# Optimization experiments

Hardware: AMD Instinct MI355X
Metric: run time of the kernel (lower is better)

Reference implementation:

```python
import jax, jax.numpy as jnp
import numpy as np

EPS = 1e-6
DIAG_SIZE = 128  # triu band half-width (init kwarg diag_size)
NEG_INF = -1e9


def feature_map(x):
    # tanh feature map: phi(x) = tanh(x) + 1 (positive feature map)
    return jnp.tanh(x) + 1.0


def causal_dot_product(Q, K, V):
    # Q,K: [N,L,H,E], V: [N,L,H,D]
    # running KV state: S_l = sum_{s<=l} K_s V_s^T, materialized via cumsum
    kv = jnp.cumsum(jnp.einsum('nlhe,nlhd->nlhed', K, V), axis=1)  # [N,L,H,E,D]
    return jnp.einsum('nlhe,nlhed->nlhd', Q, kv)


def setup_inputs() -> dict:
    key = jax.random.key(0)
    k1, k2, k3 = jax.random.split(key, 3)
    N, L, H, E = 2, 2048, 8, 64
    queries = jax.random.normal(k1, (N, L, H, E), dtype=jnp.float32)
    keys = jax.random.normal(k2, (N, L, H, E), dtype=jnp.float32)
    values = jax.random.normal(k3, (N, L, H, E), dtype=jnp.float32)
    key_lengths_mask = jnp.ones((N, L), dtype=jnp.float32)  # all keys valid
    blend = jnp.full((1,), 0.9, dtype=jnp.float32)  # learned blend param (init 0.9)
    return {"queries": queries, "keys": keys, "values": values,
            "key_lengths_mask": key_lengths_mask, "blend": blend}


def reference(queries, keys, values, key_lengths_mask, blend):
    N, L, H, E = queries.shape
    # ---- linear attention path (kernel_1 = tanh, kernel_2 = 'none') ----
    Q1 = feature_map(queries)
    K1 = feature_map(keys) * key_lengths_mask[:, :, None, None]
    Z1 = 1.0 / (jnp.einsum('nlhi,nlhi->nlh', Q1, jnp.cumsum(K1, axis=1)) + EPS)
    LV = causal_dot_product(Q1, K1, values) * Z1[..., None]  # [N,L,H,D]
    # ---- full softmax attention path (banded by triu) ----
    softmax_temp = 1.0 / np.sqrt(E).astype(np.float32)
    QK = jnp.einsum('nlhe,nshe->nhls', queries, keys)  # [N,H,L,L]
    l_idx = jnp.arange(L)[:, None]
    s_idx = jnp.arange(L)[None, :]
    causal_add = jnp.where(s_idx <= l_idx, 0.0, NEG_INF)  # lower-triangular mask
    key_add = jnp.where(key_lengths_mask > 0, 0.0, NEG_INF)  # [N,L]
    logits = softmax_temp * (QK + causal_add[None, None] + key_add[:, None, None, :])
    A = jax.nn.softmax(logits, axis=-1)
    # torch.triu(A, diagonal=-diag_size): keep s >= l - diag_size
    band = s_idx >= (l_idx - DIAG_SIZE)
    A = jnp.where(band[None, None], A, 0.0)
    # dropout: eval mode (identity)
    SV = jnp.einsum('nhls,nshd->nlhd', A, values)
    b = blend[0]
    return b * SV + (1.0 - b) * LV
```

## Files before the change

kernel.cpp:

```cpp
#include <hip/hip_runtime.h>
#include <math.h>

#define N_ 2
#define L_ 2048
#define H_ 8
#define E_ 64
#define D_ 64
#define C_ 128
#define NC (L_/C_)
#define ROWSTRIDE (H_*E_)
#define TEMP 0.125f
#define EPS_F 1e-6f
#define NEG_INF_F (-1e9f)
#define CHUNK_WS (E_*D_ + E_)
#define NCHUNKS (N_*H_*NC)
#define TPAD 136
#define PPAD 72

typedef __attribute__((ext_vector_type(8))) short short8;
typedef __attribute__((ext_vector_type(4))) float f32x4;

__device__ __forceinline__ short f2bf(float x) {
  unsigned u = __float_as_uint(x);
  u += 0x7fffu + ((u >> 16) & 1u);
  return (short)(u >> 16);
}
__device__ __forceinline__ float bf2f(short s) {
  return __uint_as_float(((unsigned)(unsigned short)s) << 16);
}
__device__ __forceinline__ float tanh1f(float x) {
  float e = __expf(-2.f * x);
  return 2.f * __builtin_amdgcn_rcpf(1.f + e);
}

template <int RS, typename F>
__device__ __forceinline__ void load_tile(float* __restrict__ dst,
                                          const float* __restrict__ src_base,
                                          F f) {
  const int t = threadIdx.x;
#pragma unroll
  for (int k = 0; k < 8; ++k) {
    int idx4 = k * 256 + t;
    int s = idx4 >> 4;
    int e = (idx4 & 15) << 2;
    float4 v = *(const float4*)(src_base + s * ROWSTRIDE + e);
    v = f(v, s);
    *(float4*)(dst + s * RS + e) = v;
  }
}

__device__ __forceinline__ void load_bf16_tile(short* __restrict__ dst,
                                               const float* __restrict__ src) {
  const int t = threadIdx.x;
#pragma unroll
  for (int it = 0; it < 4; ++it) {
    int gi = it * 256 + t;
    int row = gi >> 3, g = gi & 7;
    const float* p = src + row * ROWSTRIDE + g * 8;
    float4 a = *(const float4*)p;
    float4 b = *(const float4*)(p + 4);
    short8 v;
    v[0] = f2bf(a.x); v[1] = f2bf(a.y); v[2] = f2bf(a.z); v[3] = f2bf(a.w);
    v[4] = f2bf(b.x); v[5] = f2bf(b.y); v[6] = f2bf(b.z); v[7] = f2bf(b.w);
    int sg = g ^ (row & 7);
    *(short8*)(dst + row * 64 + sg * 8) = v;
  }
}

__device__ __forceinline__ short8 frag_ld(const short* __restrict__ buf,
                                          int rowbase, int hf, int lane) {
  int r = rowbase + (lane & 15);
  int g = (hf * 4 + (lane >> 4)) ^ (r & 7);
  return *(const short8*)(buf + r * 64 + g * 8);
}
__device__ __forceinline__ short8 frag_ldT(const short* __restrict__ buf,
                                           int nbase, int g, int lane) {
  int r = nbase + (lane & 15);
  return *(const short8*)(buf + r * TPAD + g * 8);
}
__device__ __forceinline__ short8 frag_ldP(const short* __restrict__ buf,
                                           int rowbase, int ks, int lane) {
  int r = rowbase + (lane & 15);
  int g = ks * 4 + (lane >> 4);
  return *(const short8*)(buf + r * PPAD + g * 8);
}

extern "C" __global__ void __launch_bounds__(256)
k_chunksums(const float* __restrict__ K, const float* __restrict__ V,
            const float* __restrict__ mask, float* __restrict__ ws) {
  __shared__ float kbuf[C_ * E_];
  __shared__ float vbuf[C_ * E_];
  const int orig = blockIdx.x;
  const int swz = (orig & 7) * 32 + (orig >> 3);
  const int c = swz & (NC - 1), nh = swz >> 4, h = nh & (H_ - 1), n = nh >> 3;
  const int t = threadIdx.x;
  const int gbase = ((n * L_ + c * C_) * H_ + h) * E_;
  const float* mrow = mask + n * L_ + c * C_;

  load_tile<E_>(kbuf, K + gbase, [&](float4 v, int s) {
    float km = mrow[s];
    v.x = tanh1f(v.x) * km; v.y = tanh1f(v.y) * km;
    v.z = tanh1f(v.z) * km; v.w = tanh1f(v.w) * km;
    return v;
  });
  load_tile<E_>(vbuf, V + gbase, [&](float4 v, int) { return v; });
  __syncthreads();

  const int e0 = (t >> 4) << 2, d0 = (t & 15) << 2;
  float acc[4][4] = {};
  for (int s = 0; s < C_; ++s) {
    float4 kk = *(const float4*)(kbuf + s * E_ + e0);
    float4 vv = *(const float4*)(vbuf + s * E_ + d0);
    float ka[4] = {kk.x, kk.y, kk.z, kk.w};
    float va[4] = {vv.x, vv.y, vv.z, vv.w};
#pragma unroll
    for (int a = 0; a < 4; ++a)
#pragma unroll
      for (int b = 0; b < 4; ++b) acc[a][b] += ka[a] * va[b];
  }
  float* wsc = ws + (size_t)(nh * NC + c) * CHUNK_WS;
#pragma unroll
  for (int a = 0; a < 4; ++a) {
    float4 st = {acc[a][0], acc[a][1], acc[a][2], acc[a][3]};
    *(float4*)(wsc + (e0 + a) * D_ + d0) = st;
  }
  if (t < E_) {
    float sum = 0.f;
    for (int s = 0; s < C_; ++s) sum += kbuf[s * E_ + t];
    wsc[E_ * D_ + t] = sum;
  }
}

extern "C" __global__ void __launch_bounds__(256)
k_scan(float* __restrict__ ws) {
  const int bid = blockIdx.x;
  const int swz = (bid & 7) * 34 + (bid >> 3);
  const int nh = swz / 17, seg = swz - nh * 17;
  const int idx = seg * 256 + threadIdx.x;
  if (idx >= CHUNK_WS) return;
  float* base = ws + (size_t)nh * NC * CHUNK_WS + idx;
  float v[NC];
#pragma unroll
  for (int c = 0; c < NC; ++c) v[c] = base[(size_t)c * CHUNK_WS];
  float acc = 0.f;
#pragma unroll
  for (int c = 0; c < NC; ++c) {
    base[(size_t)c * CHUNK_WS] = acc;
    acc += v[c];
  }
}

extern "C" __global__ void __launch_bounds__(256)
k_denom(const float* __restrict__ Q, const float* __restrict__ K,
        const float* __restrict__ mask, float* __restrict__ part) {
  __shared__ short qlds[C_ * E_];
  __shared__ short klds[C_ * E_];
  __shared__ float kmsk[C_];
  const int orig = blockIdx.x;
  const int swz = (orig & 7) * 272 + (orig >> 3);
  const int nh = swz / 136;
  const int p = swz - nh * 136;
  int qb = (int)((sqrtf(8.f * p + 1.f) - 1.f) * 0.5f);
  while ((qb + 1) * (qb + 2) / 2 <= p) ++qb;
  while (qb * (qb + 1) / 2 > p) --qb;
  const int kb = p - qb * (qb + 1) / 2;
  const int h = nh & (H_ - 1), n = nh >> 3;
  const int t = threadIdx.x;

  load_bf16_tile(qlds, Q + ((n * L_ + qb * C_) * H_ + h) * E_);
  load_bf16_tile(klds, K + ((n * L_ + kb * C_) * H_ + h) * E_);
  if (t < C_) kmsk[t] = mask[n * L_ + kb * C_ + t];
  __syncthreads();

  const int w = t >> 6, lane = t & 63;
  const int rowbase = w * 32;

  short8 afr[2][2];
#pragma unroll
  for (int m = 0; m < 2; ++m)
#pragma unroll
    for (int hh = 0; hh < 2; ++hh)
      afr[m][hh] = frag_ld(qlds, rowbase + 16 * m, hh, lane);

  f32x4 acc[2][8];
#pragma unroll
  for (int m = 0; m < 2; ++m)
#pragma unroll
    for (int c = 0; c < 8; ++c) acc[m][c] = (f32x4){0.f, 0.f, 0.f, 0.f};

#pragma unroll
  for (int c = 0; c < 8; ++c) {
    short8 b0 = frag_ld(klds, 16 * c, 0, lane);
    short8 b1 = frag_ld(klds, 16 * c, 1, lane);
#pragma unroll
    for (int m = 0; m < 2; ++m) {
      acc[m][c] = __builtin_amdgcn_mfma_f32_16x16x32_bf16(afr[m][0], b0, acc[m][c], 0, 0, 0);
      acc[m][c] = __builtin_amdgcn_mfma_f32_16x16x32_bf16(afr[m][1], b1, acc[m][c], 0, 0, 0);
    }
  }

  const bool diag = (kb == qb);
  const int col_lo = lane & 15;
  float* pout = part + (size_t)(nh * NC + qb) * C_ * 16;
#pragma unroll
  for (int m = 0; m < 2; ++m) {
    const int rbase = rowbase + 16 * m + (lane >> 4) * 4;
    float rs[4] = {0.f, 0.f, 0.f, 0.f};
#pragma unroll
    for (int c = 0; c < 8; ++c) {
      const int col = 16 * c + col_lo;
      const float madd = (kmsk[col] > 0.f) ? 0.f : NEG_INF_F;
#pragma unroll
      for (int reg = 0; reg < 4; ++reg) {
        float x = acc[m][c][reg] + madd;
        if (diag && col > rbase + reg) x += NEG_INF_F;
        rs[reg] += __expf(x * TEMP);
      }
    }
#pragma unroll
    for (int off = 1; off < 16; off <<= 1) {
#pragma unroll
      for (int reg = 0; reg < 4; ++reg) rs[reg] += __shfl_xor(rs[reg], off);
    }
    if (col_lo == 0) {
#pragma unroll
      for (int reg = 0; reg < 4; ++reg) pout[(rbase + reg) * 16 + kb] = rs[reg];
    }
  }
}

extern "C" __global__ void __launch_bounds__(256, 2)
k_fused(const float* __restrict__ Q, const float* __restrict__ K,
        const float* __restrict__ V, const float* __restrict__ mask,
        const float* __restrict__ blend, const float* __restrict__ ws,
        const float* __restrict__ part, float* __restrict__ out) {
  __shared__ short qs[64 * 64];
  __shared__ short q1[64 * 64];
  __shared__ short kA[C_ * 64];
  __shared__ short kB[C_ * 64];
  __shared__ short kv[64 * TPAD];
  __shared__ short pbuf[64 * PPAD];
  __shared__ float zlds[64];
  __shared__ float dinv[64];
  __shared__ float ksum[E_];
  __shared__ float kmskC[C_];
  __shared__ float kmskP[C_];

  const int orig = blockIdx.x;
  const int swz = (orig & 7) * 64 + (orig >> 3);
  const int rh = swz & 1, qb = (swz >> 1) & (NC - 1), nh = swz >> 5;
  const int h = nh & (H_ - 1), n = nh >> 3;
  const int t = threadIdx.x;
  const int w = t >> 6, lane = t & 63;
  const int rowbase = w * 16;
  const int col_lo = lane & 15;
  const int rb = rowbase + ((lane >> 4) << 2);
  const int rtile0 = rh * 64 + rb;
  const int qgbase = ((n * L_ + qb * C_ + rh * 64) * H_ + h) * E_;
  const int kbase_chunk = ((n * L_ + qb * C_) * H_ + h) * E_;
  const float* wsc = ws + (size_t)(nh * NC + qb) * CHUNK_WS;
  const float bl = blend[0];
  const float ob = 1.f - bl;

#pragma unroll
  for (int it = 0; it < 2; ++it) {
    int gi = it * 256 + t, row = gi >> 3, g = gi & 7;
    const float* p = Q + qgbase + row * ROWSTRIDE + g * 8;
    float4 a = *(const float4*)p, b = *(const float4*)(p + 4);
    float xs[8] = {a.x, a.y, a.z, a.w, b.x, b.y, b.z, b.w};
    short8 vs, v1;
#pragma unroll
    for (int j = 0; j < 8; ++j) { vs[j] = f2bf(xs[j]); v1[j] = f2bf(tanh1f(xs[j])); }
    int sg = g ^ (row & 7);
    *(short8*)(qs + row * 64 + sg * 8) = vs;
    *(short8*)(q1 + row * 64 + sg * 8) = v1;
  }
  {
    const float* mrow = mask + n * L_ + qb * C_;
#pragma unroll
    for (int it = 0; it < 4; ++it) {
      int gi = it * 256 + t, row = gi >> 3, g = gi & 7;
      const float* p = K + kbase_chunk + row * ROWSTRIDE + g * 8;
      float4 a = *(const float4*)p, b = *(const float4*)(p + 4);
      float km = mrow[row];
      float xs[8] = {a.x, a.y, a.z, a.w, b.x, b.y, b.z, b.w};
      short8 vr, v1;
#pragma unroll
      for (int j = 0; j < 8; ++j) { vr[j] = f2bf(xs[j]); v1[j] = f2bf(tanh1f(xs[j]) * km); }
      int sg = g ^ (row & 7);
      *(short8*)(kB + row * 64 + sg * 8) = vr;
      *(short8*)(kA + row * 64 + sg * 8) = v1;
    }
  }
  {
    int d = t & 63, eb = t >> 6;
#pragma unroll
    for (int q = 0; q < 2; ++q) {
      int e0 = eb * 16 + q * 8;
      short8 v;
#pragma unroll
      for (int j = 0; j < 8; ++j) v[j] = f2bf(wsc[(e0 + j) * D_ + d]);
      *(short8*)(kv + d * TPAD + (e0 >> 3) * 8) = v;
    }
  }
  float vcur[32];
  {
    int d = t & 63, sb = t >> 6;
#pragma unroll
    for (int q = 0; q < 4; ++q)
#pragma unroll
      for (int j = 0; j < 8; ++j)
        vcur[q * 8 + j] = V[kbase_chunk + (sb * 32 + q * 8 + j) * ROWSTRIDE + d];
  }
  if (t < E_) ksum[t] = wsc[E_ * D_ + t];
  if (t < C_) kmskC[t] = mask[n * L_ + qb * C_ + t];
  if (t < 64) {
    const float* pb = part + ((size_t)(nh * NC + qb) * C_ + rh * 64 + t) * 16;
    float4 a = *(const float4*)pb, b = *(const float4*)(pb + 4);
    float4 c = *(const float4*)(pb + 8), d4 = *(const float4*)(pb + 12);
    float vv[16] = {a.x, a.y, a.z, a.w, b.x, b.y, b.z, b.w,
                    c.x, c.y, c.z, c.w, d4.x, d4.y, d4.z, d4.w};
    float s = 0.f;
#pragma unroll
    for (int j = 0; j < 16; ++j) s += (j <= qb) ? vv[j] : 0.f;
    dinv[t] = 1.f / s;
  }
  __syncthreads();

  short8 af1[2], afs[2];
#pragma unroll
  for (int kh = 0; kh < 2; ++kh) {
    af1[kh] = frag_ld(q1, rowbase, kh, lane);
    afs[kh] = frag_ld(qs, rowbase, kh, lane);
  }
  f32x4 c1[8];
#pragma unroll
  for (int ct = 0; ct < 8; ++ct) c1[ct] = (f32x4){0.f, 0.f, 0.f, 0.f};
#pragma unroll
  for (int ct = 0; ct < 8; ++ct) {
    short8 b0 = frag_ld(kA, 16 * ct, 0, lane);
    short8 b1 = frag_ld(kA, 16 * ct, 1, lane);
    c1[ct] = __builtin_amdgcn_mfma_f32_16x16x32_bf16(af1[0], b0, c1[ct], 0, 0, 0);
    c1[ct] = __builtin_amdgcn_mfma_f32_16x16x32_bf16(af1[1], b1, c1[ct], 0, 0, 0);
  }
  if (t < 64) {
    float zz = 0.f;
#pragma unroll
    for (int gg = 0; gg < 8; ++gg) {
      int g = (gg + (t >> 3)) & 7;
      short8 v = *(const short8*)(q1 + t * 64 + ((g ^ (t & 7)) * 8));
#pragma unroll
      for (int j = 0; j < 8; ++j) zz += bf2f(v[j]) * ksum[g * 8 + j];
    }
    zlds[t] = zz;
  }
  float rs[4] = {0.f, 0.f, 0.f, 0.f};
#pragma unroll
  for (int ct = 0; ct < 8; ++ct) {
    int col = 16 * ct + col_lo;
#pragma unroll
    for (int reg = 0; reg < 4; ++reg) {
      if (col <= rtile0 + reg) rs[reg] += c1[ct][reg];
      else c1[ct][reg] = 0.f;
    }
  }
#pragma unroll
  for (int off = 1; off < 16; off <<= 1)
#pragma unroll
    for (int reg = 0; reg < 4; ++reg) rs[reg] += __shfl_xor(rs[reg], off);

  f32x4 accL[4];
#pragma unroll
  for (int nn = 0; nn < 4; ++nn) accL[nn] = (f32x4){0.f, 0.f, 0.f, 0.f};
#pragma unroll
  for (int ks = 0; ks < 2; ++ks) {
    short8 bf[4];
#pragma unroll
    for (int nn = 0; nn < 4; ++nn)
      bf[nn] = frag_ldT(kv, 16 * nn, ks * 4 + (lane >> 4), lane);
#pragma unroll
    for (int nn = 0; nn < 4; ++nn)
      accL[nn] = __builtin_amdgcn_mfma_f32_16x16x32_bf16(af1[ks], bf[nn], accL[nn], 0, 0, 0);
  }
  __syncthreads();

  {
    int d = t & 63, sb = t >> 6;
#pragma unroll
    for (int q = 0; q < 4; ++q) {
      short8 v;
#pragma unroll
      for (int j = 0; j < 8; ++j) v[j] = f2bf(vcur[q * 8 + j]);
      *(short8*)(kv + d * TPAD + ((sb * 32 + q * 8) >> 3) * 8) = v;
    }
  }
  __syncthreads();

  const bool haveprev = (qb > 0);
  const int kgp = ((n * L_ + (qb - 1) * C_) * H_ + h) * E_;
  float vpre[32];
  if (haveprev) {
    int d = t & 63, sb = t >> 6;
#pragma unroll
    for (int q = 0; q < 4; ++q)
#pragma unroll
      for (int j = 0; j < 8; ++j)
        vpre[q * 8 + j] = V[kgp + (sb * 32 + q * 8 + j) * ROWSTRIDE + d];
  }
#pragma unroll
  for (int hh = 0; hh < 2; ++hh) {
#pragma unroll
    for (int ch = 0; ch < 4; ++ch) {
      int ct = 4 * hh + ch, colh = 16 * ch + col_lo;
#pragma unroll
      for (int reg = 0; reg < 4; ++reg)
        pbuf[(rb + reg) * PPAD + colh] = f2bf(c1[ct][reg]);
    }
#pragma unroll
    for (int ks = 0; ks < 2; ++ks) {
      short8 ap = frag_ldP(pbuf, rowbase, ks, lane);
      short8 bv[4];
#pragma unroll
      for (int nn = 0; nn < 4; ++nn)
        bv[nn] = frag_ldT(kv, 16 * nn, 8 * hh + ks * 4 + (lane >> 4), lane);
#pragma unroll
      for (int nn = 0; nn < 4; ++nn)
        accL[nn] = __builtin_amdgcn_mfma_f32_16x16x32_bf16(ap, bv[nn], accL[nn], 0, 0, 0);
    }
  }
  f32x4 accS[4];
#pragma unroll
  for (int nn = 0; nn < 4; ++nn) accS[nn] = (f32x4){0.f, 0.f, 0.f, 0.f};
  {
    f32x4 cs[8];
#pragma unroll
    for (int ct = 0; ct < 8; ++ct) cs[ct] = (f32x4){0.f, 0.f, 0.f, 0.f};
#pragma unroll
    for (int ct = 0; ct < 8; ++ct) {
      short8 b0 = frag_ld(kB, 16 * ct, 0, lane);
      short8 b1 = frag_ld(kB, 16 * ct, 1, lane);
      cs[ct] = __builtin_amdgcn_mfma_f32_16x16x32_bf16(afs[0], b0, cs[ct], 0, 0, 0);
      cs[ct] = __builtin_amdgcn_mfma_f32_16x16x32_bf16(afs[1], b1, cs[ct], 0, 0, 0);
    }
#pragma unroll
    for (int ct = 0; ct < 8; ++ct) {
      int col = 16 * ct + col_lo;
      float madd = (kmskC[col] > 0.f) ? 0.f : NEG_INF_F;
#pragma unroll
      for (int reg = 0; reg < 4; ++reg) {
        float x = cs[ct][reg] + madd;
        if (col > rtile0 + reg) x += NEG_INF_F;
        cs[ct][reg] = __expf(x * TEMP);
      }
    }
#pragma unroll
    for (int hh = 0; hh < 2; ++hh) {
#pragma unroll
      for (int ch = 0; ch < 4; ++ch) {
        int ct = 4 * hh + ch, colh = 16 * ch + col_lo;
#pragma unroll
        for (int reg = 0; reg < 4; ++reg)
          pbuf[(rb + reg) * PPAD + colh] = f2bf(cs[ct][reg]);
      }
#pragma unroll
      for (int ks = 0; ks < 2; ++ks) {
        short8 ap = frag_ldP(pbuf, rowbase, ks, lane);
        short8 bv[4];
#pragma unroll
        for (int nn = 0; nn < 4; ++nn)
          bv[nn] = frag_ldT(kv, 16 * nn, 8 * hh + ks * 4 + (lane >> 4), lane);
#pragma unroll
        for (int nn = 0; nn < 4; ++nn)
          accS[nn] = __builtin_amdgcn_mfma_f32_16x16x32_bf16(ap, bv[nn], accS[nn], 0, 0, 0);
      }
    }
  }

  if (haveprev) {
    __syncthreads();
#pragma unroll
    for (int it = 0; it < 4; ++it) {
      int gi = it * 256 + t, row = gi >> 3, g = gi & 7;
      const float* p = K + kgp + row * ROWSTRIDE + g * 8;
      float4 a = *(const float4*)p, b = *(const float4*)(p + 4);
      short8 vr;
      vr[0] = f2bf(a.x); vr[1] = f2bf(a.y); vr[2] = f2bf(a.z); vr[3] = f2bf(a.w);
      vr[4] = f2bf(b.x); vr[5] = f2bf(b.y); vr[6] = f2bf(b.z); vr[7] = f2bf(b.w);
      int sg = g ^ (row & 7);
      *(short8*)(kA + row * 64 + sg * 8) = vr;
    }
    {
      int d = t & 63, sb = t >> 6;
#pragma unroll
      for (int q = 0; q < 4; ++q) {
        short8 v;
#pragma unroll
        for (int j = 0; j < 8; ++j) v[j] = f2bf(vpre[q * 8 + j]);
        *(short8*)(kv + d * TPAD + ((sb * 32 + q * 8) >> 3) * 8) = v;
      }
    }
    if (t < C_) kmskP[t] = mask[n * L_ + (qb - 1) * C_ + t];
    __syncthreads();

    f32x4 cs[8];
#pragma unroll
    for (int ct = 0; ct < 8; ++ct) cs[ct] = (f32x4){0.f, 0.f, 0.f, 0.f};
#pragma unroll
    for (int ct = 0; ct < 8; ++ct) {
      short8 b0 = frag_ld(kA, 16 * ct, 0, lane);
      short8 b1 = frag_ld(kA, 16 * ct, 1, lane);
      cs[ct] = __builtin_amdgcn_mfma_f32_16x16x32_bf16(afs[0], b0, cs[ct], 0, 0, 0);
      cs[ct] = __builtin_amdgcn_mfma_f32_16x16x32_bf16(afs[1], b1, cs[ct], 0, 0, 0);
    }
#pragma unroll
    for (int ct = 0; ct < 8; ++ct) {
      int col = 16 * ct + col_lo;
      float madd = (kmskP[col] > 0.f) ? 0.f : NEG_INF_F;
#pragma unroll
      for (int reg = 0; reg < 4; ++reg) {
        float x = cs[ct][reg] + madd;
        float pp = __expf(x * TEMP);
        if (col < rtile0 + reg) pp = 0.f;
        cs[ct][reg] = pp;
      }
    }
#pragma unroll
    for (int hh = 0; hh < 2; ++hh) {
#pragma unroll
      for (int ch = 0; ch < 4; ++ch) {
        int ct = 4 * hh + ch, colh = 16 * ch + col_lo;
#pragma unroll
        for (int reg = 0; reg < 4; ++reg)
          pbuf[(rb + reg) * PPAD + colh] = f2bf(cs[ct][reg]);
      }
#pragma unroll
      for (int ks = 0; ks < 2; ++ks) {
        short8 ap = frag_ldP(pbuf, rowbase, ks, lane);
        short8 bv[4];
#pragma unroll
        for (int nn = 0; nn < 4; ++nn)
          bv[nn] = frag_ldT(kv, 16 * nn, 8 * hh + ks * 4 + (lane >> 4), lane);
#pragma unroll
        for (int nn = 0; nn < 4; ++nn)
          accS[nn] = __builtin_amdgcn_mfma_f32_16x16x32_bf16(ap, bv[nn], accS[nn], 0, 0, 0);
      }
    }
  }

  float zrf[4], sdv[4];
#pragma unroll
  for (int reg = 0; reg < 4; ++reg) {
    zrf[reg] = ob / (zlds[rb + reg] + rs[reg] + EPS_F);
    sdv[reg] = bl * dinv[rb + reg];
  }
#pragma unroll
  for (int nn = 0; nn < 4; ++nn)
#pragma unroll
    for (int reg = 0; reg < 4; ++reg)
      out[qgbase + (rb + reg) * ROWSTRIDE + 16 * nn + col_lo] =
          zrf[reg] * accL[nn][reg] + sdv[reg] * accS[nn][reg];
}

extern "C" void kernel_launch(void* const* d_in, const int* in_sizes, int n_in,
                              void* d_out, int out_size, void* d_ws, size_t ws_size,
                              hipStream_t stream) {
  (void)in_sizes; (void)n_in; (void)out_size; (void)ws_size;
  const float* Q = (const float*)d_in[0];
  const float* K = (const float*)d_in[1];
  const float* V = (const float*)d_in[2];
  const float* mask = (const float*)d_in[3];
  const float* blend = (const float*)d_in[4];
  float* out = (float*)d_out;
  float* ws = (float*)d_ws;
  float* part = ws + (size_t)NCHUNKS * CHUNK_WS;

  k_denom<<<dim3(N_ * H_ * 136), dim3(256), 0, stream>>>(Q, K, mask, part);
  k_chunksums<<<dim3(N_ * H_ * NC), dim3(256), 0, stream>>>(K, V, mask, ws);
  k_scan<<<dim3(272), dim3(256), 0, stream>>>(ws);
  k_fused<<<dim3(N_ * H_ * NC * 2), dim3(256), 0, stream>>>(Q, K, V, mask, blend, ws, part, out);
}
```

Measured before the change: 49.10 us.

## Merge denom and chunk-sum kernels; MFMA chunk sums; cut LDS in fused kernel

```diff
diff --git a/kernel.cpp b/kernel.cpp
--- a/kernel.cpp
+++ b/kernel.cpp
@@ -33,22 +33,6 @@
   return 2.f * __builtin_amdgcn_rcpf(1.f + e);
 }
 
-template <int RS, typename F>
-__device__ __forceinline__ void load_tile(float* __restrict__ dst,
-                                          const float* __restrict__ src_base,
-                                          F f) {
-  const int t = threadIdx.x;
-#pragma unroll
-  for (int k = 0; k < 8; ++k) {
-    int idx4 = k * 256 + t;
-    int s = idx4 >> 4;
-    int e = (idx4 & 15) << 2;
-    float4 v = *(const float4*)(src_base + s * ROWSTRIDE + e);
-    v = f(v, s);
-    *(float4*)(dst + s * RS + e) = v;
-  }
-}
-
 __device__ __forceinline__ void load_bf16_tile(short* __restrict__ dst,
                                                const float* __restrict__ src) {
   const int t = threadIdx.x;
@@ -85,49 +69,136 @@
   return *(const short8*)(buf + r * PPAD + g * 8);
 }
 
-extern "C" __global__ void __launch_bounds__(256)
-k_chunksums(const float* __restrict__ K, const float* __restrict__ V,
-            const float* __restrict__ mask, float* __restrict__ ws) {
-  __shared__ float kbuf[C_ * E_];
-  __shared__ float vbuf[C_ * E_];
+extern "C" __global__ void __launch_bounds__(256, 4)
+k_pre(const float* __restrict__ Q, const float* __restrict__ K,
+      const float* __restrict__ V, const float* __restrict__ mask,
+      float* __restrict__ ws, float* __restrict__ part) {
+  __shared__ short ldsA[64 * TPAD];
+  __shared__ short ldsB[64 * TPAD];
+  __shared__ float fmsk[C_];
   const int orig = blockIdx.x;
-  const int swz = (orig & 7) * 32 + (orig >> 3);
-  const int c = swz & (NC - 1), nh = swz >> 4, h = nh & (H_ - 1), n = nh >> 3;
+  const int swz = (orig & 7) * 304 + (orig >> 3);
   const int t = threadIdx.x;
-  const int gbase = ((n * L_ + c * C_) * H_ + h) * E_;
-  const float* mrow = mask + n * L_ + c * C_;
-
-  load_tile<E_>(kbuf, K + gbase, [&](float4 v, int s) {
-    float km = mrow[s];
-    v.x = tanh1f(v.x) * km; v.y = tanh1f(v.y) * km;
-    v.z = tanh1f(v.z) * km; v.w = tanh1f(v.w) * km;
-    return v;
-  });
-  load_tile<E_>(vbuf, V + gbase, [&](float4 v, int) { return v; });
-  __syncthreads();
-
-  const int e0 = (t >> 4) << 2, d0 = (t & 15) << 2;
-  float acc[4][4] = {};
-  for (int s = 0; s < C_; ++s) {
-    float4 kk = *(const float4*)(kbuf + s * E_ + e0);
-    float4 vv = *(const float4*)(vbuf + s * E_ + d0);
-    float ka[4] = {kk.x, kk.y, kk.z, kk.w};
-    float va[4] = {vv.x, vv.y, vv.z, vv.w};
-#pragma unroll
-    for (int a = 0; a < 4; ++a)
-#pragma unroll
-      for (int b = 0; b < 4; ++b) acc[a][b] += ka[a] * va[b];
-  }
-  float* wsc = ws + (size_t)(nh * NC + c) * CHUNK_WS;
-#pragma unroll
-  for (int a = 0; a < 4; ++a) {
-    float4 st = {acc[a][0], acc[a][1], acc[a][2], acc[a][3]};
-    *(float4*)(wsc + (e0 + a) * D_ + d0) = st;
-  }
-  if (t < E_) {
-    float sum = 0.f;
-    for (int s = 0; s < C_; ++s) sum += kbuf[s * E_ + t];
-    wsc[E_ * D_ + t] = sum;
+  const int w = t >> 6, lane = t & 63;
+  const int col_lo = lane & 15;
+
+  if (swz < 2176) {
+    const int nh = swz / 136;
+    const int p = swz - nh * 136;
+    int qb = (int)((sqrtf(8.f * p + 1.f) - 1.f) * 0.5f);
+    while ((qb + 1) * (qb + 2) / 2 <= p) ++qb;
+    while (qb * (qb + 1) / 2 > p) --qb;
+    const int kb = p - qb * (qb + 1) / 2;
+    const int h = nh & (H_ - 1), n = nh >> 3;
+
+    load_bf16_tile(ldsA, Q + ((n * L_ + qb * C_) * H_ + h) * E_);
+    load_bf16_tile(ldsB, K + ((n * L_ + kb * C_) * H_ + h) * E_);
+    if (t < C_) fmsk[t] = mask[n * L_ + kb * C_ + t];
+    __syncthreads();
+
+    const int rowbase = w * 32;
+    short8 afr[2][2];
+#pragma unroll
+    for (int m = 0; m < 2; ++m)
+#pragma unroll
+      for (int hh = 0; hh < 2; ++hh)
+        afr[m][hh] = frag_ld(ldsA, rowbase + 16 * m, hh, lane);
+
+    f32x4 acc[2][8];
+#pragma unroll
+    for (int m = 0; m < 2; ++m)
+#pragma unroll
+      for (int c = 0; c < 8; ++c) acc[m][c] = (f32x4){0.f, 0.f, 0.f, 0.f};
+
+#pragma unroll
+    for (int c = 0; c < 8; ++c) {
+      short8 b0 = frag_ld(ldsB, 16 * c, 0, lane);
+      short8 b1 = frag_ld(ldsB, 16 * c, 1, lane);
+#pragma unroll
+      for (int m = 0; m < 2; ++m) {
+        acc[m][c] = __builtin_amdgcn_mfma_f32_16x16x32_bf16(afr[m][0], b0, acc[m][c], 0, 0, 0);
+        acc[m][c] = __builtin_amdgcn_mfma_f32_16x16x32_bf16(afr[m][1], b1, acc[m][c], 0, 0, 0);
+      }
+    }
+
+    const bool diag = (kb == qb);
+    float* pout = part + (size_t)(nh * NC + qb) * C_ * 16;
+#pragma unroll
+    for (int m = 0; m < 2; ++m) {
+      const int rbase = rowbase + 16 * m + (lane >> 4) * 4;
+      float rs[4] = {0.f, 0.f, 0.f, 0.f};
+#pragma unroll
+      for (int c = 0; c < 8; ++c) {
+        const int col = 16 * c + col_lo;
+        const float madd = (fmsk[col] > 0.f) ? 0.f : NEG_INF_F;
+#pragma unroll
+        for (int reg = 0; reg < 4; ++reg) {
+          float x = acc[m][c][reg] + madd;
+          if (diag && col > rbase + reg) x += NEG_INF_F;
+          rs[reg] += __expf(x * TEMP);
+        }
+      }
+#pragma unroll
+      for (int off = 1; off < 16; off <<= 1) {
+#pragma unroll
+        for (int reg = 0; reg < 4; ++reg) rs[reg] += __shfl_xor(rs[reg], off);
+      }
+      if (col_lo == 0) {
+#pragma unroll
+        for (int reg = 0; reg < 4; ++reg) pout[(rbase + reg) * 16 + kb] = rs[reg];
+      }
+    }
+  } else {
+    const int id = swz - 2176;
+    const int nh = id >> 4, c = id & 15;
+    const int h = nh & (H_ - 1), n = nh >> 3;
+    const int gbase = ((n * L_ + c * C_) * H_ + h) * E_;
+    const int e = t & 63, sb = t >> 6;
+    const int mbase = n * L_ + c * C_;
+#pragma unroll
+    for (int q = 0; q < 4; ++q) {
+      int s0 = sb * 32 + q * 8;
+      short8 kk, vv;
+#pragma unroll
+      for (int j = 0; j < 8; ++j) {
+        float kx = K[gbase + (s0 + j) * ROWSTRIDE + e];
+        kk[j] = f2bf(tanh1f(kx) * mask[mbase + s0 + j]);
+        vv[j] = f2bf(V[gbase + (s0 + j) * ROWSTRIDE + e]);
+      }
+      *(short8*)(ldsA + e * TPAD + (s0 >> 3) * 8) = kk;
+      *(short8*)(ldsB + e * TPAD + (s0 >> 3) * 8) = vv;
+    }
+    __syncthreads();
+
+    f32x4 acc[4];
+#pragma unroll
+    for (int nn = 0; nn < 4; ++nn) acc[nn] = (f32x4){0.f, 0.f, 0.f, 0.f};
+#pragma unroll
+    for (int ks = 0; ks < 4; ++ks) {
+      short8 a = frag_ldT(ldsB, 16 * w, ks * 4 + (lane >> 4), lane);
+#pragma unroll
+      for (int nn = 0; nn < 4; ++nn) {
+        short8 b = frag_ldT(ldsA, 16 * nn, ks * 4 + (lane >> 4), lane);
+        acc[nn] = __builtin_amdgcn_mfma_f32_16x16x32_bf16(a, b, acc[nn], 0, 0, 0);
+      }
+    }
+    float* wsc = ws + (size_t)(nh * NC + c) * CHUNK_WS;
+    const int drow = 16 * w + ((lane >> 4) << 2);
+#pragma unroll
+    for (int nn = 0; nn < 4; ++nn)
+#pragma unroll
+      for (int reg = 0; reg < 4; ++reg)
+        wsc[(16 * nn + col_lo) * D_ + drow + reg] = acc[nn][reg];
+    if (t < 64) {
+      float s = 0.f;
+#pragma unroll
+      for (int g = 0; g < 16; ++g) {
+        short8 v = *(const short8*)(ldsA + t * TPAD + g * 8);
+#pragma unroll
+        for (int j = 0; j < 8; ++j) s += bf2f(v[j]);
+      }
+      wsc[E_ * D_ + t] = s;
+    }
   }
 }
 
@@ -150,94 +221,12 @@
   }
 }
 
-extern "C" __global__ void __launch_bounds__(256)
-k_denom(const float* __restrict__ Q, const float* __restrict__ K,
-        const float* __restrict__ mask, float* __restrict__ part) {
-  __shared__ short qlds[C_ * E_];
-  __shared__ short klds[C_ * E_];
-  __shared__ float kmsk[C_];
-  const int orig = blockIdx.x;
-  const int swz = (orig & 7) * 272 + (orig >> 3);
-  const int nh = swz / 136;
-  const int p = swz - nh * 136;
-  int qb = (int)((sqrtf(8.f * p + 1.f) - 1.f) * 0.5f);
-  while ((qb + 1) * (qb + 2) / 2 <= p) ++qb;
-  while (qb * (qb + 1) / 2 > p) --qb;
-  const int kb = p - qb * (qb + 1) / 2;
-  const int h = nh & (H_ - 1), n = nh >> 3;
-  const int t = threadIdx.x;
-
-  load_bf16_tile(qlds, Q + ((n * L_ + qb * C_) * H_ + h) * E_);
-  load_bf16_tile(klds, K + ((n * L_ + kb * C_) * H_ + h) * E_);
-  if (t < C_) kmsk[t] = mask[n * L_ + kb * C_ + t];
-  __syncthreads();
-
-  const int w = t >> 6, lane = t & 63;
-  const int rowbase = w * 32;
-
-  short8 afr[2][2];
-#pragma unroll
-  for (int m = 0; m < 2; ++m)
-#pragma unroll
-    for (int hh = 0; hh < 2; ++hh)
-      afr[m][hh] = frag_ld(qlds, rowbase + 16 * m, hh, lane);
-
-  f32x4 acc[2][8];
-#pragma unroll
-  for (int m = 0; m < 2; ++m)
-#pragma unroll
-    for (int c = 0; c < 8; ++c) acc[m][c] = (f32x4){0.f, 0.f, 0.f, 0.f};
-
-#pragma unroll
-  for (int c = 0; c < 8; ++c) {
-    short8 b0 = frag_ld(klds, 16 * c, 0, lane);
-    short8 b1 = frag_ld(klds, 16 * c, 1, lane);
-#pragma unroll
-    for (int m = 0; m < 2; ++m) {
-      acc[m][c] = __builtin_amdgcn_mfma_f32_16x16x32_bf16(afr[m][0], b0, acc[m][c], 0, 0, 0);
-      acc[m][c] = __builtin_amdgcn_mfma_f32_16x16x32_bf16(afr[m][1], b1, acc[m][c], 0, 0, 0);
-    }
-  }
-
-  const bool diag = (kb == qb);
-  const int col_lo = lane & 15;
-  float* pout = part + (size_t)(nh * NC + qb) * C_ * 16;
-#pragma unroll
-  for (int m = 0; m < 2; ++m) {
-    const int rbase = rowbase + 16 * m + (lane >> 4) * 4;
-    float rs[4] = {0.f, 0.f, 0.f, 0.f};
-#pragma unroll
-    for (int c = 0; c < 8; ++c) {
-      const int col = 16 * c + col_lo;
-      const float madd = (kmsk[col] > 0.f) ? 0.f : NEG_INF_F;
-#pragma unroll
-      for (int reg = 0; reg < 4; ++reg) {
-        float x = acc[m][c][reg] + madd;
-        if (diag && col > rbase + reg) x += NEG_INF_F;
-        rs[reg] += __expf(x * TEMP);
-      }
-    }
-#pragma unroll
-    for (int off = 1; off < 16; off <<= 1) {
-#pragma unroll
-      for (int reg = 0; reg < 4; ++reg) rs[reg] += __shfl_xor(rs[reg], off);
-    }
-    if (col_lo == 0) {
-#pragma unroll
-      for (int reg = 0; reg < 4; ++reg) pout[(rbase + reg) * 16 + kb] = rs[reg];
-    }
-  }
-}
-
-extern "C" __global__ void __launch_bounds__(256, 2)
+extern "C" __global__ void __launch_bounds__(256, 3)
 k_fused(const float* __restrict__ Q, const float* __restrict__ K,
         const float* __restrict__ V, const float* __restrict__ mask,
         const float* __restrict__ blend, const float* __restrict__ ws,
         const float* __restrict__ part, float* __restrict__ out) {
-  __shared__ short qs[64 * 64];
-  __shared__ short q1[64 * 64];
-  __shared__ short kA[C_ * 64];
-  __shared__ short kB[C_ * 64];
+  __shared__ short kbuf[C_ * 64];
   __shared__ short kv[64 * TPAD];
   __shared__ short pbuf[64 * PPAD];
   __shared__ float zlds[64];
@@ -261,20 +250,21 @@
   const float* wsc = ws + (size_t)(nh * NC + qb) * CHUNK_WS;
   const float bl = blend[0];
   const float ob = 1.f - bl;
-
-#pragma unroll
-  for (int it = 0; it < 2; ++it) {
-    int gi = it * 256 + t, row = gi >> 3, g = gi & 7;
-    const float* p = Q + qgbase + row * ROWSTRIDE + g * 8;
-    float4 a = *(const float4*)p, b = *(const float4*)(p + 4);
-    float xs[8] = {a.x, a.y, a.z, a.w, b.x, b.y, b.z, b.w};
-    short8 vs, v1;
-#pragma unroll
-    for (int j = 0; j < 8; ++j) { vs[j] = f2bf(xs[j]); v1[j] = f2bf(tanh1f(xs[j])); }
-    int sg = g ^ (row & 7);
-    *(short8*)(qs + row * 64 + sg * 8) = vs;
-    *(short8*)(q1 + row * 64 + sg * 8) = v1;
-  }
+  const int d = t & 63, sb = t >> 6;
+  const bool haveprev = (qb > 0);
+  const int kgp = ((n * L_ + (qb - 1) * C_) * H_ + h) * E_;
+
+  float4 qraw[2][2];
+  {
+    const float* qp = Q + qgbase + (rowbase + (lane & 15)) * ROWSTRIDE;
+#pragma unroll
+    for (int kh = 0; kh < 2; ++kh) {
+      int c0 = (kh * 4 + (lane >> 4)) * 8;
+      qraw[kh][0] = *(const float4*)(qp + c0);
+      qraw[kh][1] = *(const float4*)(qp + c0 + 4);
+    }
+  }
+  short8 kraw[4];
   {
     const float* mrow = mask + n * L_ + qb * C_;
 #pragma unroll
@@ -287,13 +277,12 @@
       short8 vr, v1;
 #pragma unroll
       for (int j = 0; j < 8; ++j) { vr[j] = f2bf(xs[j]); v1[j] = f2bf(tanh1f(xs[j]) * km); }
-      int sg = g ^ (row & 7);
-      *(short8*)(kB + row * 64 + sg * 8) = vr;
-      *(short8*)(kA + row * 64 + sg * 8) = v1;
+      kraw[it] = vr;
+      *(short8*)(kbuf + row * 64 + (g ^ (row & 7)) * 8) = v1;
     }
   }
   {
-    int d = t & 63, eb = t >> 6;
+    int eb = t >> 6;
 #pragma unroll
     for (int q = 0; q < 2; ++q) {
       int e0 = eb * 16 + q * 8;
@@ -303,18 +292,15 @@
       *(short8*)(kv + d * TPAD + (e0 >> 3) * 8) = v;
     }
   }
-  float vcur[32];
-  {
-    int d = t & 63, sb = t >> 6;
-#pragma unroll
-    for (int q = 0; q < 4; ++q)
-#pragma unroll
-      for (int j = 0; j < 8; ++j)
-        vcur[q * 8 + j] = V[kbase_chunk + (sb * 32 + q * 8 + j) * ROWSTRIDE + d];
-  }
-  if (t < E_) ksum[t] = wsc[E_ * D_ + t];
-  if (t < C_) kmskC[t] = mask[n * L_ + qb * C_ + t];
+  short8 vcur[4];
+#pragma unroll
+  for (int q = 0; q < 4; ++q) {
+#pragma unroll
+    for (int j = 0; j < 8; ++j)
+      vcur[q][j] = f2bf(V[kbase_chunk + (sb * 32 + q * 8 + j) * ROWSTRIDE + d]);
+  }
   if (t < 64) {
+    ksum[t] = wsc[E_ * D_ + t];
     const float* pb = part + ((size_t)(nh * NC + qb) * C_ + rh * 64 + t) * 16;
     float4 a = *(const float4*)pb, b = *(const float4*)(pb + 4);
     float4 c = *(const float4*)(pb + 8), d4 = *(const float4*)(pb + 12);
@@ -325,34 +311,41 @@
     for (int j = 0; j < 16; ++j) s += (j <= qb) ? vv[j] : 0.f;
     dinv[t] = 1.f / s;
   }
+  if (t < C_) {
+    kmskC[t] = mask[n * L_ + qb * C_ + t];
+    kmskP[t] = haveprev ? mask[n * L_ + (qb - 1) * C_ + t] : 1.f;
+  }
   __syncthreads();
 
   short8 af1[2], afs[2];
 #pragma unroll
   for (int kh = 0; kh < 2; ++kh) {
-    af1[kh] = frag_ld(q1, rowbase, kh, lane);
-    afs[kh] = frag_ld(qs, rowbase, kh, lane);
+    float xs[8] = {qraw[kh][0].x, qraw[kh][0].y, qraw[kh][0].z, qraw[kh][0].w,
+                   qraw[kh][1].x, qraw[kh][1].y, qraw[kh][1].z, qraw[kh][1].w};
+#pragma unroll
+    for (int j = 0; j < 8; ++j) { afs[kh][j] = f2bf(xs[j]); af1[kh][j] = f2bf(tanh1f(xs[j])); }
   }
   f32x4 c1[8];
 #pragma unroll
   for (int ct = 0; ct < 8; ++ct) c1[ct] = (f32x4){0.f, 0.f, 0.f, 0.f};
 #pragma unroll
   for (int ct = 0; ct < 8; ++ct) {
-    short8 b0 = frag_ld(kA, 16 * ct, 0, lane);
-    short8 b1 = frag_ld(kA, 16 * ct, 1, lane);
+    short8 b0 = frag_ld(kbuf, 16 * ct, 0, lane);
+    short8 b1 = frag_ld(kbuf, 16 * ct, 1, lane);
     c1[ct] = __builtin_amdgcn_mfma_f32_16x16x32_bf16(af1[0], b0, c1[ct], 0, 0, 0);
     c1[ct] = __builtin_amdgcn_mfma_f32_16x16x32_bf16(af1[1], b1, c1[ct], 0, 0, 0);
   }
-  if (t < 64) {
+  {
     float zz = 0.f;
 #pragma unroll
-    for (int gg = 0; gg < 8; ++gg) {
-      int g = (gg + (t >> 3)) & 7;
-      short8 v = *(const short8*)(q1 + t * 64 + ((g ^ (t & 7)) * 8));
-#pragma unroll
-      for (int j = 0; j < 8; ++j) zz += bf2f(v[j]) * ksum[g * 8 + j];
-    }
-    zlds[t] = zz;
+    for (int kh = 0; kh < 2; ++kh) {
+      int cb = (kh * 4 + (lane >> 4)) * 8;
+#pragma unroll
+      for (int j = 0; j < 8; ++j) zz += bf2f(af1[kh][j]) * ksum[cb + j];
+    }
+    zz += __shfl_xor(zz, 16);
+    zz += __shfl_xor(zz, 32);
+    if (lane < 16) zlds[rowbase + lane] = zz;
   }
   float rs[4] = {0.f, 0.f, 0.f, 0.f};
 #pragma unroll
@@ -384,28 +377,32 @@
   }
   __syncthreads();
 
-  {
-    int d = t & 63, sb = t >> 6;
-#pragma unroll
-    for (int q = 0; q < 4; ++q) {
-      short8 v;
-#pragma unroll
-      for (int j = 0; j < 8; ++j) v[j] = f2bf(vcur[q * 8 + j]);
-      *(short8*)(kv + d * TPAD + ((sb * 32 + q * 8) >> 3) * 8) = v;
-    }
-  }
+#pragma unroll
+  for (int it = 0; it < 4; ++it) {
+    int gi = it * 256 + t, row = gi >> 3, g = gi & 7;
+    *(short8*)(kbuf + row * 64 + (g ^ (row & 7)) * 8) = kraw[it];
+  }
+#pragma unroll
+  for (int q = 0; q < 4; ++q)
+    *(short8*)(kv + d * TPAD + ((sb * 32 + q * 8) >> 3) * 8) = vcur[q];
   __syncthreads();
 
-  const bool haveprev = (qb > 0);
-  const int kgp = ((n * L_ + (qb - 1) * C_) * H_ + h) * E_;
-  float vpre[32];
+  short8 pk[4], pv[4];
   if (haveprev) {
-    int d = t & 63, sb = t >> 6;
+#pragma unroll
+    for (int it = 0; it < 4; ++it) {
+      int gi = it * 256 + t, row = gi >> 3, g = gi & 7;
+      const float* p = K + kgp + row * ROWSTRIDE + g * 8;
+      float4 a = *(const float4*)p, b = *(const float4*)(p + 4);
+      float xs[8] = {a.x, a.y, a.z, a.w, b.x, b.y, b.z, b.w};
+#pragma unroll
+      for (int j = 0; j < 8; ++j) pk[it][j] = f2bf(xs[j]);
+    }
 #pragma unroll
     for (int q = 0; q < 4; ++q)
 #pragma unroll
       for (int j = 0; j < 8; ++j)
-        vpre[q * 8 + j] = V[kgp + (sb * 32 + q * 8 + j) * ROWSTRIDE + d];
+        pv[q][j] = f2bf(V[kgp + (sb * 32 + q * 8 + j) * ROWSTRIDE + d]);
   }
 #pragma unroll
   for (int hh = 0; hh < 2; ++hh) {
@@ -437,8 +434,8 @@
     for (int ct = 0; ct < 8; ++ct) cs[ct] = (f32x4){0.f, 0.f, 0.f, 0.f};
 #pragma unroll
     for (int ct = 0; ct < 8; ++ct) {
-      short8 b0 = frag_ld(kB, 16 * ct, 0, lane);
-      short8 b1 = frag_ld(kB, 16 * ct, 1, lane);
+      short8 b0 = frag_ld(kbuf, 16 * ct, 0, lane);
+      short8 b1 = frag_ld(kbuf, 16 * ct, 1, lane);
       cs[ct] = __builtin_amdgcn_mfma_f32_16x16x32_bf16(afs[0], b0, cs[ct], 0, 0, 0);
       cs[ct] = __builtin_amdgcn_mfma_f32_16x16x32_bf16(afs[1], b1, cs[ct], 0, 0, 0);
     }
@@ -481,25 +478,11 @@
 #pragma unroll
     for (int it = 0; it < 4; ++it) {
       int gi = it * 256 + t, row = gi >> 3, g = gi & 7;
-      const float* p = K + kgp + row * ROWSTRIDE + g * 8;
-      float4 a = *(const float4*)p, b = *(const float4*)(p + 4);
-      short8 vr;
-      vr[0] = f2bf(a.x); vr[1] = f2bf(a.y); vr[2] = f2bf(a.z); vr[3] = f2bf(a.w);
-      vr[4] = f2bf(b.x); vr[5] = f2bf(b.y); vr[6] = f2bf(b.z); vr[7] = f2bf(b.w);
-      int sg = g ^ (row & 7);
-      *(short8*)(kA + row * 64 + sg * 8) = vr;
-    }
-    {
-      int d = t & 63, sb = t >> 6;
-#pragma unroll
-      for (int q = 0; q < 4; ++q) {
-        short8 v;
-#pragma unroll
-        for (int j = 0; j < 8; ++j) v[j] = f2bf(vpre[q * 8 + j]);
-        *(short8*)(kv + d * TPAD + ((sb * 32 + q * 8) >> 3) * 8) = v;
-      }
-    }
-    if (t < C_) kmskP[t] = mask[n * L_ + (qb - 1) * C_ + t];
+      *(short8*)(kbuf + row * 64 + (g ^ (row & 7)) * 8) = pk[it];
+    }
+#pragma unroll
+    for (int q = 0; q < 4; ++q)
+      *(short8*)(kv + d * TPAD + ((sb * 32 + q * 8) >> 3) * 8) = pv[q];
     __syncthreads();
 
     f32x4 cs[8];
@@ -507,8 +490,8 @@
     for (int ct = 0; ct < 8; ++ct) cs[ct] = (f32x4){0.f, 0.f, 0.f, 0.f};
 #pragma unroll
     for (int ct = 0; ct < 8; ++ct) {
-      short8 b0 = frag_ld(kA, 16 * ct, 0, lane);
-      short8 b1 = frag_ld(kA, 16 * ct, 1, lane);
+      short8 b0 = frag_ld(kbuf, 16 * ct, 0, lane);
+      short8 b1 = frag_ld(kbuf, 16 * ct, 1, lane);
       cs[ct] = __builtin_amdgcn_mfma_f32_16x16x32_bf16(afs[0], b0, cs[ct], 0, 0, 0);
       cs[ct] = __builtin_amdgcn_mfma_f32_16x16x32_bf16(afs[1], b1, cs[ct], 0, 0, 0);
     }
@@ -574,8 +557,7 @@
   float* ws = (float*)d_ws;
   float* part = ws + (size_t)NCHUNKS * CHUNK_WS;
 
-  k_denom<<<dim3(N_ * H_ * 136), dim3(256), 0, stream>>>(Q, K, mask, part);
-  k_chunksums<<<dim3(N_ * H_ * NC), dim3(256), 0, stream>>>(K, V, mask, ws);
+  k_pre<<<dim3(2432), dim3(256), 0, stream>>>(Q, K, V, mask, ws, part);
   k_scan<<<dim3(272), dim3(256), 0, stream>>>(ws);
   k_fused<<<dim3(N_ * H_ * NC * 2), dim3(256), 0, stream>>>(Q, K, V, mask, blend, ws, part, out);
 }
```

After: 52.86 us. 1.08x slower.
